# Optimization experiments

Measured on AMD Instinct MI355X. Metric: run time of the kernel, lower is better.

## Reference

```python
import jax, jax.numpy as jnp
import numpy as np

FS = 100.0  # sampling_rate


def _csd(x, NF):
    # CrossSpectralDensity: per-batch, all-pairs cross-correlation (torch conv1d padding='same'),
    # then rfft over time and mean over the F*F pair axis.
    B, T, F = x.shape
    left = (T - 1) // 2                      # torch 'same' padding: left=floor, right=ceil
    xpad = jnp.pad(x, ((0, 0), (left, T - 1 - left), (0, 0)))

    def per_batch(xp_b, x_b):
        # xp_b: (Tp,F) padded signals, x_b: (T,F) kernels
        lhs = xp_b.T[:, None, :]             # (F_i, 1, Tp)  signals as batch
        rhs = x_b.T[:, None, :]              # (F_j, 1, T)   kernels as out-channels
        # lax conv = cross-correlation (no flip), matching torch conv1d
        return jax.lax.conv_general_dilated(lhs, rhs, (1,), 'VALID')  # (F_i, F_j, T)

    convs = jax.vmap(per_batch)(xpad, x)                    # (B, F, F, T)
    convs = jnp.transpose(convs, (0, 3, 1, 2)).reshape(B, T, F * F)  # pair index i*F+j
    cf = jnp.fft.rfft(convs, axis=1, norm='ortho')[:, :NF, :]
    return cf.mean(axis=-1, keepdims=True)                  # (B, NF, 1)


def reference(x, W_proj, b_proj, W_gate, b_gate, mag_w, mag_b, phase_w, phase_b, ln_gamma, ln_beta):
    B, H, F = x.shape
    NF = mag_w.shape[0]                     # = H//2 + 1 (threshold = fs/2 keeps all freqs)
    hid = W_proj.shape[1]

    fft = jnp.fft.rfft(x, axis=1, norm='ortho')[:, :NF, :]  # (B, NF, F) complex
    fft = fft + _csd(x, NF)

    mag = jnp.abs(fft)
    ang = jnp.angle(fft)
    freqs = jnp.arange(NF, dtype=x.dtype) * (FS / H)        # rfftfreq(H, 1/FS)
    ff = jnp.concatenate([
        jnp.stack([mag, jnp.sin(ang), jnp.cos(ang)], axis=-1),
        jnp.broadcast_to(freqs[None, :, None, None], (B, NF, F, 1)),
    ], axis=-1)                                             # (B, NF, F, 4)

    # per-freq projection layers all share one weight (ModuleList of the same module)
    proj = jax.nn.relu(jnp.einsum('bnfk,kh->bnfh', ff, W_proj) + b_proj)  # (B, NF, F, hid)

    # cat over freq along last dim -> (B, F, NF*hid), element [.., i*hid+h] = proj[:, i, :, h]
    flat = jnp.transpose(proj, (0, 2, 1, 3)).reshape(B, F, NF * hid)
    g = flat @ W_gate + b_gate                              # (B, F, NF)
    g = g * jax.nn.sigmoid(g)                               # SimpleGate (SiLU)
    w = jnp.transpose(jax.nn.sigmoid(g), (0, 2, 1))         # (B, NF, F)

    # Complexifier per frequency (distinct weights per freq); proj is already >=0 (relu idempotent)
    m = jax.nn.relu(jnp.einsum('bnfh,nh->bnf', proj, mag_w) + mag_b[None, :, None])
    ph = 2.0 * jnp.pi * jax.nn.sigmoid(jnp.einsum('bnfh,nh->bnf', proj, phase_w) + phase_b[None, :, None])
    new_fft = m * jnp.cos(ph) + 1j * (m * jnp.sin(ph))      # (B, NF, F) complex

    wf = w * new_fft + (1.0 - w) * fft
    wf = jnp.pad(wf, ((0, 0), (0, H // 2 + 1 - NF), (0, 0)))  # no-op here (NF == H//2+1)
    recon = jnp.fft.irfft(wf, axis=1, norm='ortho')         # (B, H, F)

    # LayerNorm(input_size) over residual
    y = recon + x
    mu = y.mean(axis=-1, keepdims=True)
    var = ((y - mu) ** 2).mean(axis=-1, keepdims=True)
    return (y - mu) / jnp.sqrt(var + 1e-5) * ln_gamma + ln_beta


def setup_inputs():
    key = jax.random.key(0)
    ks = jax.random.split(key, 12)
    B, H, F, HID = 128, 512, 16, 64
    NF = H // 2 + 1  # 257
    s = 0.05
    return {
        'x': jax.random.normal(ks[0], (B, H, F), jnp.float32),
        'W_proj': jax.random.normal(ks[1], (4, HID), jnp.float32) * s,
        'b_proj': jax.random.normal(ks[2], (HID,), jnp.float32) * s,
        'W_gate': jax.random.normal(ks[3], (NF * HID, NF), jnp.float32) * 0.01,
        'b_gate': jax.random.normal(ks[4], (NF,), jnp.float32) * s,
        'mag_w': jax.random.normal(ks[5], (NF, HID), jnp.float32) * s,
        'mag_b': jax.random.normal(ks[6], (NF,), jnp.float32) * s,
        'phase_w': jax.random.normal(ks[7], (NF, HID), jnp.float32) * s,
        'phase_b': jax.random.normal(ks[8], (NF,), jnp.float32) * s,
        'ln_gamma': jnp.ones((F,), jnp.float32),
        'ln_beta': jnp.zeros((F,), jnp.float32),
    }
```

## Files before the change

### kernel.cpp

```cpp
#include <hip/hip_runtime.h>


#define NF_ 257
#define NKB 514
#define FRAGS 263168
#define SPK 16
#define SORTHO 0.04419417382f

typedef __attribute__((ext_vector_type(8))) short short8;
typedef __attribute__((ext_vector_type(4))) float floatx4;

__device__ __forceinline__ unsigned int f2bf(float x) {
  union { float f; unsigned int u; } v; v.f = x;
  return (v.u + 0x7FFFu + ((v.u >> 16) & 1u)) >> 16;
}
__device__ __forceinline__ float bf2f(unsigned int u16) {
  union { unsigned int u; float f; } v; v.u = u16 << 16;
  return v.f;
}

__global__ __launch_bounds__(256) void k_prep(const float* __restrict__ x,
                                              const float* __restrict__ Wg,
                                              float* __restrict__ csd,
                                              unsigned short* __restrict__ Bf,
                                              unsigned short* __restrict__ TWf,
                                              unsigned short* __restrict__ ITWf) {
  __shared__ float sl[768];
  __shared__ float ac[257];
  __shared__ float red[4];
  const int tid = threadIdx.x;
  const int blk = blockIdx.x;

  if (blk < 128) {
    const int bb = blk;
    for (int t = tid; t < 768; t += 256) {
      float v = 0.f;
      if (t < 512) {
        const float4* xp = (const float4*)(x + (bb * 512 + t) * 16);
        float4 a = xp[0], b = xp[1], c = xp[2], d = xp[3];
        v = a.x + a.y + a.z + a.w + b.x + b.y + b.z + b.w +
            c.x + c.y + c.z + c.w + d.x + d.y + d.z + d.w;
      }
      sl[t] = v;
    }
    __syncthreads();
    {
      float a0 = 0.f, a1 = 0.f, a2 = 0.f, a3 = 0.f;
      for (int tau = 0; tau < 512; tau += 4) {
        float4 u = *(const float4*)&sl[tau];
        a0 = fmaf(u.x, sl[tau + tid], a0);
        a1 = fmaf(u.y, sl[tau + tid + 1], a1);
        a2 = fmaf(u.z, sl[tau + tid + 2], a2);
        a3 = fmaf(u.w, sl[tau + tid + 3], a3);
      }
      ac[tid] = (a0 + a1) + (a2 + a3);
    }
    {
      float p = sl[tid] * sl[tid + 256];
#pragma unroll
      for (int off = 32; off; off >>= 1) p += __shfl_down(p, off);
      if ((tid & 63) == 0) red[tid >> 6] = p;
    }
    __syncthreads();
    if (tid == 0) ac[256] = red[0] + red[1] + red[2] + red[3];
    __syncthreads();
    const float S1 = SORTHO / 256.f;
    const int k = tid;
    float sth, cth;
    __sincosf((float)k * 0.01227184630f, &sth, &cth);
    float c = 1.f, s = 0.f, re = 0.f, im = 0.f;
    float re256 = 0.f, sg = 1.f;
    for (int t = 0; t < 512; ++t) {
      int d = t - 255;
      float ov = ac[d < 0 ? -d : d];
      re = fmaf(ov, c, re);
      im = fmaf(-ov, s, im);
      re256 = fmaf(ov, sg, re256);
      sg = -sg;
      float nc = fmaf(c, cth, -s * sth);
      s = fmaf(s, cth, c * sth);
      c = nc;
    }
    *(float2*)(csd + (bb * NF_ + k) * 2) = make_float2(re * S1, im * S1);
    if (tid == 0)
      *(float2*)(csd + (bb * NF_ + 256) * 2) = make_float2(re256 * S1, 0.f);
    return;
  }

  if (blk < 2698) {
    const int slot = (blk - 128) * 256 + tid;
    const int nblk = slot / 32896;
    const int rem = slot - nblk * 32896;
    const int kb = rem >> 6, lane = rem & 63;
    const int n = nblk * 16 + (lane & 15);
    const int k0 = kb * 32 + (lane >> 4) * 8;
    unsigned int w[4];
#pragma unroll
    for (int jp = 0; jp < 4; ++jp) {
      float v0 = (n < NF_) ? Wg[(k0 + jp * 2) * NF_ + n] : 0.f;
      float v1 = (n < NF_) ? Wg[(k0 + jp * 2 + 1) * NF_ + n] : 0.f;
      w[jp] = f2bf(v0) | (f2bf(v1) << 16);
    }
    *(uint4*)(Bf + (size_t)slot * 8) = make_uint4(w[0], w[1], w[2], w[3]);
    return;
  }

  if (blk < 2834) {
    const int slot = (blk - 2698) * 256 + tid;
    const int tile = slot >> 10, rem = slot & 1023;
    const int ks = rem >> 6, quad = (rem >> 4) & 3, l15 = rem & 15;
    const int grow = tile * 16 + l15;
    unsigned int pk[4];
#pragma unroll
    for (int jp = 0; jp < 4; ++jp) {
      float v0 = 0.f, v1 = 0.f;
      if (grow < 514) {
        const int k = grow >> 1;
        const int t0 = ks * 32 + quad * 8 + jp * 2;
        float s0, c0, s1, c1;
        __sincosf((float)((k * t0) & 511) * 0.01227184630f, &s0, &c0);
        __sincosf((float)((k * (t0 + 1)) & 511) * 0.01227184630f, &s1, &c1);
        v0 = (grow & 1) ? -s0 * SORTHO : c0 * SORTHO;
        v1 = (grow & 1) ? -s1 * SORTHO : c1 * SORTHO;
      }
      pk[jp] = f2bf(v0) | (f2bf(v1) << 16);
    }
    *(uint4*)(TWf + slot * 8) = make_uint4(pk[0], pk[1], pk[2], pk[3]);
    return;
  }

  {
    const int slot = (blk - 2834) * 256 + tid;
    const int tile = slot / 1088, rem = slot % 1088;
    const int ks = rem >> 6, sub = rem & 63;
    const int quad = sub >> 4, l15 = sub & 15;
    const int t = tile * 16 + l15;
    unsigned int pk[4];
#pragma unroll
    for (int jp = 0; jp < 4; ++jp) {
      float v0 = 0.f, v1 = 0.f;
#pragma unroll
      for (int h = 0; h < 2; ++h) {
        const int kidx = ks * 32 + quad * 8 + jp * 2 + h;
        float v = 0.f;
        if (kidx < 514) {
          const int k = kidx >> 1;
          const float hw = (k == 0 || k == 256) ? SORTHO : 2.f * SORTHO;
          float s, c;
          __sincosf((float)((k * t) & 511) * 0.01227184630f, &s, &c);
          v = (kidx & 1) ? -s * hw : c * hw;
        }
        if (h == 0) v0 = v; else v1 = v;
      }
      pk[jp] = f2bf(v0) | (f2bf(v1) << 16);
    }
    *(uint4*)(ITWf + slot * 8) = make_uint4(pk[0], pk[1], pk[2], pk[3]);
  }
}

__global__ __launch_bounds__(512) void k_fftg(const float* __restrict__ x,
                                              const unsigned short* __restrict__ TWf,
                                              const float* __restrict__ csd,
                                              float* __restrict__ fftc) {
  __shared__ __align__(16) unsigned short Xs[16 * 512];
  const int tid = threadIdx.x, mh = blockIdx.x, bb = blockIdx.y;
#pragma unroll
  for (int it = 0; it < 16; ++it) {
    int e = it * 512 + tid;
    int f = e & 15, t = e >> 4;
    float val = x[(bb * 512 + t) * 16 + f];
    Xs[f * 512 + (((t >> 3) ^ (f & 7)) * 8) + (t & 7)] = (unsigned short)f2bf(val);
  }
  __syncthreads();
  const int lane = tid & 63, wave = tid >> 6;
  const int l15 = lane & 15, quad = lane >> 4;
  floatx4 acc0 = {0,0,0,0}, acc1 = {0,0,0,0}, acc2 = {0,0,0,0};
  const int g0 = mh * 17 + wave, g1 = g0 + 8, g2 = mh * 17 + 16;
#pragma unroll
  for (int ks = 0; ks < 16; ++ks) {
    short8 bf = *(const short8*)&Xs[l15 * 512 + (((ks * 4 + quad) ^ (l15 & 7)) * 8)];
    short8 af0 = *(const short8*)(TWf + g0 * 8192 + ks * 512 + quad * 128 + l15 * 8);
    short8 af1 = *(const short8*)(TWf + g1 * 8192 + ks * 512 + quad * 128 + l15 * 8);
    acc0 = __builtin_amdgcn_mfma_f32_16x16x32_bf16(af0, bf, acc0, 0, 0, 0);
    acc1 = __builtin_amdgcn_mfma_f32_16x16x32_bf16(af1, bf, acc1, 0, 0, 0);
    if (wave == 0) {
      short8 af2 = *(const short8*)(TWf + g2 * 8192 + ks * 512 + quad * 128 + l15 * 8);
      acc2 = __builtin_amdgcn_mfma_f32_16x16x32_bf16(af2, bf, acc2, 0, 0, 0);
    }
  }
#pragma unroll
  for (int i = 0; i < 3; ++i) {
    if (i == 2 && wave != 0) break;
    const int g = (i == 0) ? g0 : (i == 1) ? g1 : g2;
    floatx4 a = (i == 0) ? acc0 : (i == 1) ? acc1 : acc2;
#pragma unroll
    for (int r = 0; r < 4; ++r) {
      const int grow = g * 16 + quad * 4 + r;
      if (grow < 514) {
        const int k = grow >> 1, ri = grow & 1;
        fftc[((bb * NF_ + k) * 16 + l15) * 2 + ri] =
            a[r] + csd[(bb * NF_ + k) * 2 + ri];
      }
    }
  }
}

__global__ __launch_bounds__(256) void k_new(const float* __restrict__ fftc,
                                             const float* __restrict__ W_proj,
                                             const float* __restrict__ b_proj,
                                             const float* __restrict__ mag_w,
                                             const float* __restrict__ mag_b,
                                             const float* __restrict__ phase_w,
                                             const float* __restrict__ phase_b,
                                             float* __restrict__ nf,
                                             unsigned short* __restrict__ Af) {
  __shared__ float wp[256], bp[64];
  const int tid = threadIdx.x;
  wp[tid] = W_proj[tid];
  if (tid < 64) bp[tid] = b_proj[tid];
  __syncthreads();
  const int idx = blockIdx.x * 256 + tid;
  const int bn = idx >> 4, f = idx & 15;
  const int n = bn % NF_, b = bn / NF_;
  float2 z = *(const float2*)(fftc + idx * 2);
  float d = z.x * z.x + z.y * z.y;
  float ir = d > 0.f ? rsqrtf(d) : 0.f;
  float mag = d * ir;
  float sn = z.y * ir;
  float cs = d > 0.f ? z.x * ir : 1.f;
  float fr = (float)n * 0.1953125f;
  float am = 0.f, ap = 0.f;
  unsigned short* abase = Af + ((size_t)b * NKB + n * 2) * 512 + f * 8;
#pragma unroll
  for (int hg = 0; hg < 8; ++hg) {
    unsigned int w[4];
#pragma unroll
    for (int j = 0; j < 8; ++j) {
      const int h = hg * 8 + j;
      float p = fmaf(mag, wp[h], fmaf(sn, wp[64 + h], fmaf(cs, wp[128 + h],
                fmaf(fr, wp[192 + h], bp[h]))));
      p = fmaxf(p, 0.f);
      am = fmaf(p, mag_w[n * 64 + h], am);
      ap = fmaf(p, phase_w[n * 64 + h], ap);
      unsigned int pb16 = f2bf(p);
      if (j & 1) w[j >> 1] |= pb16 << 16; else w[j >> 1] = pb16;
    }
    *(uint4*)(abase + (hg >> 2) * 512 + (hg & 3) * 128) =
        make_uint4(w[0], w[1], w[2], w[3]);
  }
  float m = fmaxf(am + mag_b[n], 0.f);
  float ph = 6.28318530718f / (1.f + __expf(-(ap + phase_b[n])));
  float sp, cp;
  __sincosf(ph, &sp, &cp);
  *(float2*)(nf + idx * 2) = make_float2(m * cp, m * sp);
}

__global__ __launch_bounds__(256, 2) void k_gemm(const unsigned short* __restrict__ Af,
                                                 const unsigned short* __restrict__ Bf,
                                                 unsigned short* __restrict__ gpart) {
  __shared__ __align__(16) unsigned short As[2][4096];
  const int tid = threadIdx.x;
  const int sp = blockIdx.x, mgg = blockIdx.y;
  const int lane = tid & 63, wv = tid >> 6;
  const int p0 = (NF_ * sp) >> 4, p1 = (NF_ * (sp + 1)) >> 4;
  const int nsteps = p1 - p0;
  const int c0 = wv * 2, c1 = wv * 2 + 1;
  const unsigned short* aSrc0 = Af + (size_t)(mgg * 4 + (c0 & 3)) * FRAGS
                                + (size_t)(p0 * 2 + (c0 >> 2)) * 512 + lane * 8;
  const unsigned short* aSrc1 = Af + (size_t)(mgg * 4 + (c1 & 3)) * FRAGS
                                + (size_t)(p0 * 2 + (c1 >> 2)) * 512 + lane * 8;
  const unsigned short* pb = Bf + (size_t)(wv * 5) * FRAGS
                             + (size_t)(p0 * 2) * 512 + lane * 8;

  floatx4 acc[4][5];
#pragma unroll
  for (int mi = 0; mi < 4; ++mi)
#pragma unroll
    for (int nn = 0; nn < 5; ++nn) acc[mi][nn] = (floatx4){0.f, 0.f, 0.f, 0.f};

  uint4 ra0 = *(const uint4*)aSrc0;
  uint4 ra1 = *(const uint4*)aSrc1;
  short8 bX[5], bY[5];
#pragma unroll
  for (int nn = 0; nn < 5; ++nn) {
    bX[nn] = *(const short8*)(pb + (size_t)nn * FRAGS);
    bY[nn] = *(const short8*)(pb + (size_t)nn * FRAGS + 512);
  }

  for (int s = 0; s < nsteps; ++s) {
    unsigned short* dst = &As[s & 1][0];
    *(uint4*)(dst + c0 * 512 + lane * 8) = ra0;
    *(uint4*)(dst + c1 * 512 + lane * 8) = ra1;
    if (s + 1 < nsteps) {
      aSrc0 += 1024; aSrc1 += 1024;
      ra0 = *(const uint4*)aSrc0;
      ra1 = *(const uint4*)aSrc1;
    }
    __builtin_amdgcn_sched_barrier(0);
    asm volatile("s_waitcnt lgkmcnt(0)" ::: "memory");
    __builtin_amdgcn_s_barrier();
    __builtin_amdgcn_sched_barrier(0);
    const unsigned short* rb = &As[s & 1][0];
    {
      short8 a0 = *(const short8*)(rb + 0 * 512 + lane * 8);
      short8 a1 = *(const short8*)(rb + 1 * 512 + lane * 8);
      short8 a2 = *(const short8*)(rb + 2 * 512 + lane * 8);
      short8 a3 = *(const short8*)(rb + 3 * 512 + lane * 8);
#pragma unroll
      for (int nn = 0; nn < 5; ++nn) {
        acc[0][nn] = __builtin_amdgcn_mfma_f32_16x16x32_bf16(a0, bX[nn], acc[0][nn], 0, 0, 0);
        acc[1][nn] = __builtin_amdgcn_mfma_f32_16x16x32_bf16(a1, bX[nn], acc[1][nn], 0, 0, 0);
        acc[2][nn] = __builtin_amdgcn_mfma_f32_16x16x32_bf16(a2, bX[nn], acc[2][nn], 0, 0, 0);
        acc[3][nn] = __builtin_amdgcn_mfma_f32_16x16x32_bf16(a3, bX[nn], acc[3][nn], 0, 0, 0);
      }
      if (s + 1 < nsteps) {
#pragma unroll
        for (int nn = 0; nn < 5; ++nn)
          bX[nn] = *(const short8*)(pb + (size_t)nn * FRAGS + 1024);
      }
    }
    {
      short8 a0 = *(const short8*)(rb + 4 * 512 + lane * 8);
      short8 a1 = *(const short8*)(rb + 5 * 512 + lane * 8);
      short8 a2 = *(const short8*)(rb + 6 * 512 + lane * 8);
      short8 a3 = *(const short8*)(rb + 7 * 512 + lane * 8);
#pragma unroll
      for (int nn = 0; nn < 5; ++nn) {
        acc[0][nn] = __builtin_amdgcn_mfma_f32_16x16x32_bf16(a0, bY[nn], acc[0][nn], 0, 0, 0);
        acc[1][nn] = __builtin_amdgcn_mfma_f32_16x16x32_bf16(a1, bY[nn], acc[1][nn], 0, 0, 0);
        acc[2][nn] = __builtin_amdgcn_mfma_f32_16x16x32_bf16(a2, bY[nn], acc[2][nn], 0, 0, 0);
        acc[3][nn] = __builtin_amdgcn_mfma_f32_16x16x32_bf16(a3, bY[nn], acc[3][nn], 0, 0, 0);
      }
      if (s + 1 < nsteps) {
#pragma unroll
        for (int nn = 0; nn < 5; ++nn)
          bY[nn] = *(const short8*)(pb + (size_t)nn * FRAGS + 1536);
        pb += 1024;
      }
    }
  }

#pragma unroll
  for (int mi = 0; mi < 4; ++mi)
#pragma unroll
    for (int nn = 0; nn < 5; ++nn) {
      unsigned int lo = f2bf(acc[mi][nn][0]) | (f2bf(acc[mi][nn][1]) << 16);
      unsigned int hi = f2bf(acc[mi][nn][2]) | (f2bf(acc[mi][nn][3]) << 16);
      *(uint2*)(gpart + ((((size_t)sp * 128 + mgg * 4 + mi) * 20) + wv * 5 + nn) * 256
                + lane * 4) = make_uint2(lo, hi);
    }
}

__global__ __launch_bounds__(512) void k_recong(const float* __restrict__ fftc,
                                                const float* __restrict__ nfb,
                                                const unsigned short* __restrict__ gpart,
                                                const float* __restrict__ b_gate,
                                                const unsigned short* __restrict__ ITWf,
                                                const float* __restrict__ x,
                                                const float* __restrict__ ln_g,
                                                const float* __restrict__ ln_b,
                                                float* __restrict__ out) {
  __shared__ __align__(16) unsigned short WFs[16 * 576];
  __shared__ float wls[16 * 257];
  const int tid = threadIdx.x, th = blockIdx.x, bb = blockIdx.y;
  const unsigned short* gpb = gpart + (size_t)bb * 5120;
  for (int t = tid; t < 1088; t += 512) {
    const int n = ((t >> 6) << 4) + (t & 15);
    if (n < NF_) {
      const int quad = (t >> 4) & 3;
      const float bg = b_gate[n];
      float g0 = bg, g1 = bg, g2 = bg, g3 = bg;
#pragma unroll
      for (int s2 = 0; s2 < SPK; ++s2) {
        uint2 v = *(const uint2*)(gpb + (size_t)s2 * 655360 + (size_t)t * 4);
        g0 += bf2f(v.x & 0xFFFFu); g1 += bf2f(v.x >> 16);
        g2 += bf2f(v.y & 0xFFFFu); g3 += bf2f(v.y >> 16);
      }
      float gv[4] = {g0, g1, g2, g3};
#pragma unroll
      for (int r = 0; r < 4; ++r) {
        float g = gv[r];
        float sg = 1.f / (1.f + __expf(-g));
        float gs = g * sg;
        wls[(quad * 4 + r) * 257 + n] = 1.f / (1.f + __expf(-gs));
      }
    }
  }
  __syncthreads();
#pragma unroll
  for (int it = 0; it < 17; ++it) {
    int e = it * 512 + tid;
    int f = e & 15, row = e >> 4;
    float val = 0.f;
    if (row < 514) {
      int k = row >> 1, ri = row & 1;
      int base = ((bb * NF_ + k) * 16 + f) * 2 + ri;
      float fz = fftc[base], nz = nfb[base];
      float wv = wls[f * 257 + k];
      val = fz + wv * (nz - fz);
    }
    WFs[f * 576 + (((row >> 3) ^ (f & 7)) * 8) + (row & 7)] = (unsigned short)f2bf(val);
  }
  __syncthreads();
  const int lane = tid & 63, wave = tid >> 6;
  const int l15 = lane & 15, quad = lane >> 4;
  const float gg = ln_g[l15], gb = ln_b[l15];
  floatx4 acc[2];
  acc[0] = (floatx4){0.f, 0.f, 0.f, 0.f};
  acc[1] = (floatx4){0.f, 0.f, 0.f, 0.f};
  const int tg0 = th * 16 + wave, tg1 = tg0 + 8;
#pragma unroll
  for (int ks = 0; ks < 17; ++ks) {
    short8 bf = *(const short8*)&WFs[l15 * 576 + (((ks * 4 + quad) ^ (l15 & 7)) * 8)];
    short8 af0 = *(const short8*)(ITWf + tg0 * 8704 + ks * 512 + quad * 128 + l15 * 8);
    short8 af1 = *(const short8*)(ITWf + tg1 * 8704 + ks * 512 + quad * 128 + l15 * 8);
    acc[0] = __builtin_amdgcn_mfma_f32_16x16x32_bf16(af0, bf, acc[0], 0, 0, 0);
    acc[1] = __builtin_amdgcn_mfma_f32_16x16x32_bf16(af1, bf, acc[1], 0, 0, 0);
  }
#pragma unroll
  for (int i = 0; i < 2; ++i) {
    const int tg = (i == 0) ? tg0 : tg1;
#pragma unroll
    for (int r = 0; r < 4; ++r) {
      const int t = tg * 16 + quad * 4 + r;
      float y = acc[i][r] + x[(bb * 512 + t) * 16 + l15];
      float s1 = y, s2 = y * y;
#pragma unroll
      for (int m = 1; m < 16; m <<= 1) {
        s1 += __shfl_xor(s1, m);
        s2 += __shfl_xor(s2, m);
      }
      float mu = s1 * 0.0625f;
      float var = s2 * 0.0625f - mu * mu;
      float rs = rsqrtf(var + 1e-5f);
      out[(bb * 512 + t) * 16 + l15] = (y - mu) * rs * gg + gb;
    }
  }
}

extern "C" void kernel_launch(void* const* d_in, const int* in_sizes, int n_in,
                              void* d_out, int out_size, void* d_ws, size_t ws_size,
                              hipStream_t stream) {
  const float* x = (const float*)d_in[0];
  const float* W_proj = (const float*)d_in[1];
  const float* b_proj = (const float*)d_in[2];
  const float* W_gate = (const float*)d_in[3];
  const float* b_gate = (const float*)d_in[4];
  const float* mag_w = (const float*)d_in[5];
  const float* mag_b = (const float*)d_in[6];
  const float* phase_w = (const float*)d_in[7];
  const float* phase_b = (const float*)d_in[8];
  const float* ln_g = (const float*)d_in[9];
  const float* ln_b = (const float*)d_in[10];
  float* out = (float*)d_out;
  float* ws = (float*)d_ws;

  float* fftc = ws;
  float* nfb = ws + 1052672;
  float* csd = ws + 2631680;
  unsigned short* Afrag = (unsigned short*)(ws + 2697472);
  unsigned short* Bfrag = (unsigned short*)(ws + 19540224);
  unsigned short* gpart = (unsigned short*)(ws + 22171904);
  unsigned short* TWf = (unsigned short*)(ws + 27414784);
  unsigned short* ITWf = (unsigned short*)(ws + 27554048);

  hipLaunchKernelGGL(k_prep, dim3(2970), dim3(256), 0, stream,
                     x, W_gate, csd, Bfrag, TWf, ITWf);
  hipLaunchKernelGGL(k_fftg, dim3(2, 128), dim3(512), 0, stream, x, TWf, csd, fftc);
  hipLaunchKernelGGL(k_new, dim3(2056), dim3(256), 0, stream, fftc, W_proj, b_proj,
                     mag_w, mag_b, phase_w, phase_b, nfb, Afrag);
  hipLaunchKernelGGL(k_gemm, dim3(16, 32), dim3(256), 0, stream, Afrag, Bfrag, gpart);
  hipLaunchKernelGGL(k_recong, dim3(2, 128), dim3(512), 0, stream, fftc, nfb, gpart,
                     b_gate, ITWf, x, ln_g, ln_b, out);
}
```

Baseline: 183.5 us.

## Compute projection activations inside GEMM instead of materializing bf16 A fragments

The GEMM kernel now reads the complex FFT values directly, computes the relu projection features in registers, converts them to bf16 and writes them to shared memory. The large intermediate A-fragment buffer is no longer written by k_new or read back by the GEMM. This removes a big global-memory round trip. In exchange the projection math is recomputed across the 16 column-split blocks and sits on the GEMM's per-step critical path, and k_new now only produces the magnitude/phase outputs.

After: 181.4 us. No clear change (-1.2%).

```diff
diff --git a/kernel.cpp b/kernel.cpp
--- a/kernel.cpp
+++ b/kernel.cpp
@@ -2,7 +2,6 @@
 
 
 #define NF_ 257
-#define NKB 514
 #define FRAGS 263168
 #define SPK 16
 #define SORTHO 0.04419417382f
@@ -212,16 +211,15 @@
                                              const float* __restrict__ mag_b,
                                              const float* __restrict__ phase_w,
                                              const float* __restrict__ phase_b,
-                                             float* __restrict__ nf,
-                                             unsigned short* __restrict__ Af) {
+                                             float* __restrict__ nf) {
   __shared__ float wp[256], bp[64];
   const int tid = threadIdx.x;
   wp[tid] = W_proj[tid];
   if (tid < 64) bp[tid] = b_proj[tid];
   __syncthreads();
   const int idx = blockIdx.x * 256 + tid;
-  const int bn = idx >> 4, f = idx & 15;
-  const int n = bn % NF_, b = bn / NF_;
+  const int bn = idx >> 4;
+  const int n = bn % NF_;
   float2 z = *(const float2*)(fftc + idx * 2);
   float d = z.x * z.x + z.y * z.y;
   float ir = d > 0.f ? rsqrtf(d) : 0.f;
@@ -230,23 +228,13 @@
   float cs = d > 0.f ? z.x * ir : 1.f;
   float fr = (float)n * 0.1953125f;
   float am = 0.f, ap = 0.f;
-  unsigned short* abase = Af + ((size_t)b * NKB + n * 2) * 512 + f * 8;
-#pragma unroll
-  for (int hg = 0; hg < 8; ++hg) {
-    unsigned int w[4];
-#pragma unroll
-    for (int j = 0; j < 8; ++j) {
-      const int h = hg * 8 + j;
-      float p = fmaf(mag, wp[h], fmaf(sn, wp[64 + h], fmaf(cs, wp[128 + h],
-                fmaf(fr, wp[192 + h], bp[h]))));
-      p = fmaxf(p, 0.f);
-      am = fmaf(p, mag_w[n * 64 + h], am);
-      ap = fmaf(p, phase_w[n * 64 + h], ap);
-      unsigned int pb16 = f2bf(p);
-      if (j & 1) w[j >> 1] |= pb16 << 16; else w[j >> 1] = pb16;
-    }
-    *(uint4*)(abase + (hg >> 2) * 512 + (hg & 3) * 128) =
-        make_uint4(w[0], w[1], w[2], w[3]);
+#pragma unroll 8
+  for (int h = 0; h < 64; ++h) {
+    float p = fmaf(mag, wp[h], fmaf(sn, wp[64 + h], fmaf(cs, wp[128 + h],
+              fmaf(fr, wp[192 + h], bp[h]))));
+    p = fmaxf(p, 0.f);
+    am = fmaf(p, mag_w[n * 64 + h], am);
+    ap = fmaf(p, phase_w[n * 64 + h], ap);
   }
   float m = fmaxf(am + mag_b[n], 0.f);
   float ph = 6.28318530718f / (1.f + __expf(-(ap + phase_b[n])));
@@ -255,20 +243,32 @@
   *(float2*)(nf + idx * 2) = make_float2(m * cp, m * sp);
 }
 
-__global__ __launch_bounds__(256, 2) void k_gemm(const unsigned short* __restrict__ Af,
+__global__ __launch_bounds__(256, 2) void k_gemm(const float* __restrict__ fftc,
+                                                 const float* __restrict__ W_proj,
+                                                 const float* __restrict__ b_proj,
                                                  const unsigned short* __restrict__ Bf,
                                                  unsigned short* __restrict__ gpart) {
   __shared__ __align__(16) unsigned short As[2][4096];
   const int tid = threadIdx.x;
   const int sp = blockIdx.x, mgg = blockIdx.y;
   const int lane = tid & 63, wv = tid >> 6;
+  const int q = lane >> 4, l15 = lane & 15;
   const int p0 = (NF_ * sp) >> 4, p1 = (NF_ * (sp + 1)) >> 4;
   const int nsteps = p1 - p0;
-  const int c0 = wv * 2, c1 = wv * 2 + 1;
-  const unsigned short* aSrc0 = Af + (size_t)(mgg * 4 + (c0 & 3)) * FRAGS
-                                + (size_t)(p0 * 2 + (c0 >> 2)) * 512 + lane * 8;
-  const unsigned short* aSrc1 = Af + (size_t)(mgg * 4 + (c1 & 3)) * FRAGS
-                                + (size_t)(p0 * 2 + (c1 >> 2)) * 512 + lane * 8;
+  const int c0 = wv * 2, c1 = c0 + 1;
+  const int kf = wv >> 1;
+  const int mi0 = (wv & 1) * 2, mi1 = mi0 + 1;
+  const int b0 = mgg * 4 + mi0, b1 = b0 + 1;
+
+  float4 w4[8]; float bpv[8];
+  const int hb = kf * 32 + q * 8;
+#pragma unroll
+  for (int j = 0; j < 8; ++j) {
+    const int h = hb + j;
+    w4[j] = make_float4(W_proj[h], W_proj[64 + h], W_proj[128 + h], W_proj[192 + h]);
+    bpv[j] = b_proj[h];
+  }
+
   const unsigned short* pb = Bf + (size_t)(wv * 5) * FRAGS
                              + (size_t)(p0 * 2) * 512 + lane * 8;
 
@@ -278,8 +278,8 @@
 #pragma unroll
     for (int nn = 0; nn < 5; ++nn) acc[mi][nn] = (floatx4){0.f, 0.f, 0.f, 0.f};
 
-  uint4 ra0 = *(const uint4*)aSrc0;
-  uint4 ra1 = *(const uint4*)aSrc1;
+  float2 z0 = *(const float2*)(fftc + ((b0 * NF_ + p0) * 16 + l15) * 2);
+  float2 z1 = *(const float2*)(fftc + ((b1 * NF_ + p0) * 16 + l15) * 2);
   short8 bX[5], bY[5];
 #pragma unroll
   for (int nn = 0; nn < 5; ++nn) {
@@ -288,14 +288,47 @@
   }
 
   for (int s = 0; s < nsteps; ++s) {
+    const int n = p0 + s;
+    const float fr = (float)n * 0.1953125f;
+    float2 zn0, zn1;
+    if (s + 1 < nsteps) {
+      zn0 = *(const float2*)(fftc + ((b0 * NF_ + n + 1) * 16 + l15) * 2);
+      zn1 = *(const float2*)(fftc + ((b1 * NF_ + n + 1) * 16 + l15) * 2);
+    }
     unsigned short* dst = &As[s & 1][0];
-    *(uint4*)(dst + c0 * 512 + lane * 8) = ra0;
-    *(uint4*)(dst + c1 * 512 + lane * 8) = ra1;
-    if (s + 1 < nsteps) {
-      aSrc0 += 1024; aSrc1 += 1024;
-      ra0 = *(const uint4*)aSrc0;
-      ra1 = *(const uint4*)aSrc1;
-    }
+    {
+      float d = z0.x * z0.x + z0.y * z0.y;
+      float ir = d > 0.f ? rsqrtf(d) : 0.f;
+      float mag = d * ir, sn = z0.y * ir;
+      float cs = d > 0.f ? z0.x * ir : 1.f;
+      unsigned int w[4];
+#pragma unroll
+      for (int j = 0; j < 8; ++j) {
+        float p = fmaf(mag, w4[j].x, fmaf(sn, w4[j].y, fmaf(cs, w4[j].z,
+                  fmaf(fr, w4[j].w, bpv[j]))));
+        p = fmaxf(p, 0.f);
+        unsigned int pb16 = f2bf(p);
+        if (j & 1) w[j >> 1] |= pb16 << 16; else w[j >> 1] = pb16;
+      }
+      *(uint4*)(dst + c0 * 512 + lane * 8) = make_uint4(w[0], w[1], w[2], w[3]);
+    }
+    {
+      float d = z1.x * z1.x + z1.y * z1.y;
+      float ir = d > 0.f ? rsqrtf(d) : 0.f;
+      float mag = d * ir, sn = z1.y * ir;
+      float cs = d > 0.f ? z1.x * ir : 1.f;
+      unsigned int w[4];
+#pragma unroll
+      for (int j = 0; j < 8; ++j) {
+        float p = fmaf(mag, w4[j].x, fmaf(sn, w4[j].y, fmaf(cs, w4[j].z,
+                  fmaf(fr, w4[j].w, bpv[j]))));
+        p = fmaxf(p, 0.f);
+        unsigned int pb16 = f2bf(p);
+        if (j & 1) w[j >> 1] |= pb16 << 16; else w[j >> 1] = pb16;
+      }
+      *(uint4*)(dst + c1 * 512 + lane * 8) = make_uint4(w[0], w[1], w[2], w[3]);
+    }
+    z0 = zn0; z1 = zn1;
     __builtin_amdgcn_sched_barrier(0);
     asm volatile("s_waitcnt lgkmcnt(0)" ::: "memory");
     __builtin_amdgcn_s_barrier();
@@ -458,18 +491,18 @@
   float* fftc = ws;
   float* nfb = ws + 1052672;
   float* csd = ws + 2631680;
-  unsigned short* Afrag = (unsigned short*)(ws + 2697472);
-  unsigned short* Bfrag = (unsigned short*)(ws + 19540224);
-  unsigned short* gpart = (unsigned short*)(ws + 22171904);
-  unsigned short* TWf = (unsigned short*)(ws + 27414784);
-  unsigned short* ITWf = (unsigned short*)(ws + 27554048);
+  unsigned short* Bfrag = (unsigned short*)(ws + 2697472);
+  unsigned short* gpart = (unsigned short*)(ws + 5329152);
+  unsigned short* TWf = (unsigned short*)(ws + 10572032);
+  unsigned short* ITWf = (unsigned short*)(ws + 10711296);
 
   hipLaunchKernelGGL(k_prep, dim3(2970), dim3(256), 0, stream,
                      x, W_gate, csd, Bfrag, TWf, ITWf);
   hipLaunchKernelGGL(k_fftg, dim3(2, 128), dim3(512), 0, stream, x, TWf, csd, fftc);
+  hipLaunchKernelGGL(k_gemm, dim3(16, 32), dim3(256), 0, stream, fftc, W_proj,
+                     b_proj, Bfrag, gpart);
   hipLaunchKernelGGL(k_new, dim3(2056), dim3(256), 0, stream, fftc, W_proj, b_proj,
-                     mag_w, mag_b, phase_w, phase_b, nfb, Afrag);
-  hipLaunchKernelGGL(k_gemm, dim3(16, 32), dim3(256), 0, stream, Afrag, Bfrag, gpart);
+                     mag_w, mag_b, phase_w, phase_b, nfb);
   hipLaunchKernelGGL(k_recong, dim3(2, 128), dim3(512), 0, stream, fftc, nfb, gpart,
                      b_gate, ITWf, x, ln_g, ln_b, out);
 }
```
